# Performance work log

Hardware: AMD Instinct MI355X
Metric: run time of the kernel (lower is better)

## Reference

```python
import jax, jax.numpy as jnp
import numpy as np


def setup_inputs() -> dict:
    key = jax.random.key(0)
    k1, = jax.random.split(key, 1)
    B, H, W, C = 16, 64, 64, 256
    x = jax.random.normal(k1, (B, H, W, C), dtype=jnp.float32)
    gamma = jnp.zeros((1,), dtype=jnp.float32)
    return {"x": x, "gamma": gamma}


def reference(x, gamma):
    B, H, W, C = x.shape
    a = x.reshape(B, H * W, C)                      # [B, HW, C]
    # aTa[b, i, j] = sum_n a[b, n, i] * a[b, n, j]  -> [B, C, C]
    aTa = jnp.einsum('bni,bnj->bij', a, a)
    attn = jax.nn.softmax(aTa, axis=-1)             # softmax over last channel axis
    # aaTa[b, n, j] = sum_i a[b, n, i] * attn[b, i, j]
    aaTa = jnp.einsum('bni,bij->bnj', a, attn)      # [B, HW, C]
    aaTa = aaTa.reshape(B, H, W, C)
    return gamma * aaTa + x
```

## Files before the change

### kernel.cpp

```cpp
#include <hip/hip_runtime.h>
#include <hip/hip_bf16.h>


#define BB 16
#define NN 4096
#define CC 256
#define SPLITK 8
#define KCHUNK (NN / SPLITK)

typedef __attribute__((ext_vector_type(4))) short short4v;
typedef __attribute__((ext_vector_type(8))) short short8v;
typedef __attribute__((ext_vector_type(4))) float floatx4;

__device__ __forceinline__ unsigned short f2bf(float f) {
    unsigned int u = __float_as_uint(f);
    u += 0x7fffu + ((u >> 16) & 1u);
    return (unsigned short)(u >> 16);
}
__device__ __forceinline__ short4v cvt4(floatx4 v) {
    short4v r;
    r[0] = (short)f2bf(v[0]); r[1] = (short)f2bf(v[1]);
    r[2] = (short)f2bf(v[2]); r[3] = (short)f2bf(v[3]);
    return r;
}

__global__ __launch_bounds__(256) void k_transpose(const float* __restrict__ x,
                                                   unsigned short* __restrict__ aT) {
    __shared__ unsigned short tile[64 * 68];
    const int b  = blockIdx.z;
    const int n0 = blockIdx.x * 64;
    const int c0 = blockIdx.y * 64;
    const int t  = threadIdx.x;
    const int q4 = (t & 15) * 4;
    const int tr = t >> 4;

    const float* xb = x + ((size_t)b * NN + n0) * CC + c0;
    for (int r = 0; r < 4; ++r) {
        int row = tr + 16 * r;
        floatx4 v = *(const floatx4*)(xb + (size_t)row * CC + q4);
        *(short4v*)&tile[row * 68 + q4] = cvt4(v);
    }
    __syncthreads();
    unsigned short* aTb = aT + ((size_t)b * CC + c0) * NN + n0;
    for (int r = 0; r < 4; ++r) {
        int c = tr + 16 * r;
        short4v v;
        v[0] = (short)tile[(q4 + 0) * 68 + c];
        v[1] = (short)tile[(q4 + 1) * 68 + c];
        v[2] = (short)tile[(q4 + 2) * 68 + c];
        v[3] = (short)tile[(q4 + 3) * 68 + c];
        *(short4v*)(aTb + (size_t)c * NN + q4) = v;
    }
}

__global__ __launch_bounds__(256) void k_gemm1(const unsigned short* __restrict__ aT,
                                               float* __restrict__ aTa) {
    __shared__ unsigned short Ap[64 * 72];
    __shared__ unsigned short Bp[64 * 72];
    const int b     = blockIdx.z >> 3;
    const int split = blockIdx.z & 7;
    const int i0 = blockIdx.x * 64;
    const int j0 = blockIdx.y * 64;
    const int t  = threadIdx.x;
    const int w  = t >> 6, l = t & 63;
    const int wm = (w >> 1) * 32, wn = (w & 1) * 32;
    const int lk = (l >> 4) * 8;
    const int lm = l & 15;
    const int sc = t >> 4;
    const int sk = (t & 15) * 4;

    const unsigned short* Abase = aT + ((size_t)b * CC + i0) * NN;
    const unsigned short* Bbase = aT + ((size_t)b * CC + j0) * NN;

    floatx4 acc[2][2] = {};
    const int kbeg = split * KCHUNK;
    for (int k0 = kbeg; k0 < kbeg + KCHUNK; k0 += 64) {
        for (int r = 0; r < 4; ++r) {
            int c = sc + 16 * r;
            *(short4v*)&Ap[c * 72 + sk] = *(const short4v*)(Abase + (size_t)c * NN + k0 + sk);
            *(short4v*)&Bp[c * 72 + sk] = *(const short4v*)(Bbase + (size_t)c * NN + k0 + sk);
        }
        __syncthreads();
        for (int ks = 0; ks < 64; ks += 32) {
            short8v af0 = *(const short8v*)&Ap[(wm + 0  + lm) * 72 + ks + lk];
            short8v af1 = *(const short8v*)&Ap[(wm + 16 + lm) * 72 + ks + lk];
            short8v bf0 = *(const short8v*)&Bp[(wn + 0  + lm) * 72 + ks + lk];
            short8v bf1 = *(const short8v*)&Bp[(wn + 16 + lm) * 72 + ks + lk];
            acc[0][0] = __builtin_amdgcn_mfma_f32_16x16x32_bf16(af0, bf0, acc[0][0], 0, 0, 0);
            acc[0][1] = __builtin_amdgcn_mfma_f32_16x16x32_bf16(af0, bf1, acc[0][1], 0, 0, 0);
            acc[1][0] = __builtin_amdgcn_mfma_f32_16x16x32_bf16(af1, bf0, acc[1][0], 0, 0, 0);
            acc[1][1] = __builtin_amdgcn_mfma_f32_16x16x32_bf16(af1, bf1, acc[1][1], 0, 0, 0);
        }
        __syncthreads();
    }
    const int orow = (l >> 4) * 4;
    for (int mt = 0; mt < 2; ++mt)
        for (int nt = 0; nt < 2; ++nt)
            for (int r = 0; r < 4; ++r) {
                int i = i0 + wm + mt * 16 + orow + r;
                int j = j0 + wn + nt * 16 + lm;
                unsafeAtomicAdd(&aTa[((size_t)b * CC + i) * CC + j], acc[mt][nt][r]);
            }
}

__global__ __launch_bounds__(256) void k_softmax(const float* __restrict__ aTa,
                                                 unsigned short* __restrict__ attnT) {
    const int w = threadIdx.x >> 6;
    const int l = threadIdx.x & 63;
    const int row = blockIdx.x * 4 + w;
    const int b = row >> 8;
    const int i = row & 255;
    const float* p = aTa + ((size_t)b * CC + i) * CC;
    float v0 = p[l], v1 = p[l + 64], v2 = p[l + 128], v3 = p[l + 192];
    float m = fmaxf(fmaxf(v0, v1), fmaxf(v2, v3));
    for (int off = 32; off >= 1; off >>= 1) m = fmaxf(m, __shfl_xor(m, off, 64));
    v0 = __expf(v0 - m); v1 = __expf(v1 - m); v2 = __expf(v2 - m); v3 = __expf(v3 - m);
    float s = v0 + v1 + v2 + v3;
    for (int off = 32; off >= 1; off >>= 1) s += __shfl_xor(s, off, 64);
    float rs = 1.0f / s;
    unsigned short* o = attnT + (size_t)b * CC * CC + i;
    o[(size_t)(l +   0) * CC] = f2bf(v0 * rs);
    o[(size_t)(l +  64) * CC] = f2bf(v1 * rs);
    o[(size_t)(l + 128) * CC] = f2bf(v2 * rs);
    o[(size_t)(l + 192) * CC] = f2bf(v3 * rs);
}

__global__ __launch_bounds__(256) void k_gemm2(const float* __restrict__ x,
                                               const unsigned short* __restrict__ attnT,
                                               const float* __restrict__ gamma,
                                               float* __restrict__ out) {
    __shared__ unsigned short At[64 * 72];
    __shared__ unsigned short Bt[64 * 72];
    const int b  = blockIdx.z;
    const int n0 = blockIdx.x * 64;
    const int j0 = blockIdx.y * 64;
    const int t  = threadIdx.x;
    const int w  = t >> 6, l = t & 63;
    const int wm = (w >> 1) * 32, wn = (w & 1) * 32;
    const int lk = (l >> 4) * 8, lm = l & 15;
    const int sc = t >> 4, sk = (t & 15) * 4;

    const float*          Abase = x + ((size_t)b * NN + n0) * CC;
    const unsigned short* Bbase = attnT + ((size_t)b * CC + j0) * CC;

    floatx4 acc[2][2] = {};
    for (int k0 = 0; k0 < CC; k0 += 64) {
        for (int r = 0; r < 4; ++r) {
            int c = sc + 16 * r;
            floatx4 av = *(const floatx4*)(Abase + (size_t)c * CC + k0 + sk);
            *(short4v*)&At[c * 72 + sk] = cvt4(av);
            *(short4v*)&Bt[c * 72 + sk] = *(const short4v*)(Bbase + (size_t)c * CC + k0 + sk);
        }
        __syncthreads();
        for (int ks = 0; ks < 64; ks += 32) {
            short8v af0 = *(const short8v*)&At[(wm + 0  + lm) * 72 + ks + lk];
            short8v af1 = *(const short8v*)&At[(wm + 16 + lm) * 72 + ks + lk];
            short8v bf0 = *(const short8v*)&Bt[(wn + 0  + lm) * 72 + ks + lk];
            short8v bf1 = *(const short8v*)&Bt[(wn + 16 + lm) * 72 + ks + lk];
            acc[0][0] = __builtin_amdgcn_mfma_f32_16x16x32_bf16(af0, bf0, acc[0][0], 0, 0, 0);
            acc[0][1] = __builtin_amdgcn_mfma_f32_16x16x32_bf16(af0, bf1, acc[0][1], 0, 0, 0);
            acc[1][0] = __builtin_amdgcn_mfma_f32_16x16x32_bf16(af1, bf0, acc[1][0], 0, 0, 0);
            acc[1][1] = __builtin_amdgcn_mfma_f32_16x16x32_bf16(af1, bf1, acc[1][1], 0, 0, 0);
        }
        __syncthreads();
    }
    const float g = gamma[0];
    const int orow = (l >> 4) * 4;
    for (int mt = 0; mt < 2; ++mt)
        for (int nt = 0; nt < 2; ++nt)
            for (int r = 0; r < 4; ++r) {
                int nr = n0 + wm + mt * 16 + orow + r;
                int j  = j0 + wn + nt * 16 + lm;
                size_t idx = ((size_t)b * NN + nr) * CC + j;
                out[idx] = g * acc[mt][nt][r] + x[idx];
            }
}

extern "C" void kernel_launch(void* const* d_in, const int* in_sizes, int n_in,
                              void* d_out, int out_size, void* d_ws, size_t ws_size,
                              hipStream_t stream) {
    const float* x     = (const float*)d_in[0];
    const float* gamma = (const float*)d_in[1];
    float* out = (float*)d_out;

    char* ws = (char*)d_ws;
    unsigned short* aT    = (unsigned short*)ws;
    float*          aTa   = (float*)(ws + (size_t)BB * CC * NN * 2);
    unsigned short* attnT = (unsigned short*)(ws + (size_t)BB * CC * NN * 2
                                                 + (size_t)BB * CC * CC * 4);

    hipMemsetAsync(aTa, 0, (size_t)BB * CC * CC * sizeof(float), stream);

    k_transpose<<<dim3(NN / 64, CC / 64, BB), 256, 0, stream>>>(x, aT);
    k_gemm1   <<<dim3(CC / 64, CC / 64, BB * SPLITK), 256, 0, stream>>>(aT, aTa);
    k_softmax <<<dim3(BB * CC / 4),          256, 0, stream>>>(aTa, attnT);
    k_gemm2   <<<dim3(NN / 64, CC / 64, BB), 256, 0, stream>>>(x, attnT, gamma, out);
}
```

Baseline: 187.3 us.

## Widen GEMM tiles to 64x256 and replace split-K atomics with partial buffers

Both GEMMs now compute a 64x256 output tile per block, with each wave owning a 64x64 sub-tile of sixteen accumulators. This cuts redundant reloads of the A operand (x is read once per row block in gemm2) and raises MFMA work per LDS load. Split-K atomics and the memset in gemm1 are replaced by writing per-split partial results to workspace, which softmax then sums. The cost is more LDS per block (about 46KB), more registers, fewer blocks in flight (512 for gemm1, 1024 for gemm2), and eightfold partial-buffer traffic for softmax to read.

```diff
diff --git a/kernel.cpp b/kernel.cpp
--- a/kernel.cpp
+++ b/kernel.cpp
@@ -54,64 +54,80 @@
 }
 
 __global__ __launch_bounds__(256) void k_gemm1(const unsigned short* __restrict__ aT,
-                                               float* __restrict__ aTa) {
+                                               float* __restrict__ part) {
     __shared__ unsigned short Ap[64 * 72];
-    __shared__ unsigned short Bp[64 * 72];
-    const int b     = blockIdx.z >> 3;
-    const int split = blockIdx.z & 7;
-    const int i0 = blockIdx.x * 64;
-    const int j0 = blockIdx.y * 64;
+    __shared__ unsigned short Bp[256 * 72];
+    const int i0    = blockIdx.x * 64;
+    const int b     = blockIdx.y;
+    const int split = blockIdx.z;
     const int t  = threadIdx.x;
     const int w  = t >> 6, l = t & 63;
-    const int wm = (w >> 1) * 32, wn = (w & 1) * 32;
     const int lk = (l >> 4) * 8;
     const int lm = l & 15;
     const int sc = t >> 4;
     const int sk = (t & 15) * 4;
 
     const unsigned short* Abase = aT + ((size_t)b * CC + i0) * NN;
-    const unsigned short* Bbase = aT + ((size_t)b * CC + j0) * NN;
-
-    floatx4 acc[2][2] = {};
+    const unsigned short* Bbase = aT + (size_t)b * CC * NN;
+
+    floatx4 acc[4][4] = {};
     const int kbeg = split * KCHUNK;
     for (int k0 = kbeg; k0 < kbeg + KCHUNK; k0 += 64) {
+        #pragma unroll
         for (int r = 0; r < 4; ++r) {
-            int c = sc + 16 * r;
-            *(short4v*)&Ap[c * 72 + sk] = *(const short4v*)(Abase + (size_t)c * NN + k0 + sk);
-            *(short4v*)&Bp[c * 72 + sk] = *(const short4v*)(Bbase + (size_t)c * NN + k0 + sk);
-        }
-        __syncthreads();
+            int i = sc + 16 * r;
+            *(short4v*)&Ap[i * 72 + sk] = *(const short4v*)(Abase + (size_t)i * NN + k0 + sk);
+        }
+        #pragma unroll
+        for (int r = 0; r < 16; ++r) {
+            int j = sc + 16 * r;
+            *(short4v*)&Bp[j * 72 + sk] = *(const short4v*)(Bbase + (size_t)j * NN + k0 + sk);
+        }
+        __syncthreads();
+        #pragma unroll
         for (int ks = 0; ks < 64; ks += 32) {
-            short8v af0 = *(const short8v*)&Ap[(wm + 0  + lm) * 72 + ks + lk];
-            short8v af1 = *(const short8v*)&Ap[(wm + 16 + lm) * 72 + ks + lk];
-            short8v bf0 = *(const short8v*)&Bp[(wn + 0  + lm) * 72 + ks + lk];
-            short8v bf1 = *(const short8v*)&Bp[(wn + 16 + lm) * 72 + ks + lk];
-            acc[0][0] = __builtin_amdgcn_mfma_f32_16x16x32_bf16(af0, bf0, acc[0][0], 0, 0, 0);
-            acc[0][1] = __builtin_amdgcn_mfma_f32_16x16x32_bf16(af0, bf1, acc[0][1], 0, 0, 0);
-            acc[1][0] = __builtin_amdgcn_mfma_f32_16x16x32_bf16(af1, bf0, acc[1][0], 0, 0, 0);
-            acc[1][1] = __builtin_amdgcn_mfma_f32_16x16x32_bf16(af1, bf1, acc[1][1], 0, 0, 0);
+            short8v af[4], bf[4];
+            #pragma unroll
+            for (int mt = 0; mt < 4; ++mt)
+                af[mt] = *(const short8v*)&Ap[(mt * 16 + lm) * 72 + ks + lk];
+            #pragma unroll
+            for (int nt = 0; nt < 4; ++nt)
+                bf[nt] = *(const short8v*)&Bp[(w * 64 + nt * 16 + lm) * 72 + ks + lk];
+            #pragma unroll
+            for (int mt = 0; mt < 4; ++mt)
+                #pragma unroll
+                for (int nt = 0; nt < 4; ++nt)
+                    acc[mt][nt] = __builtin_amdgcn_mfma_f32_16x16x32_bf16(af[mt], bf[nt], acc[mt][nt], 0, 0, 0);
         }
         __syncthreads();
     }
     const int orow = (l >> 4) * 4;
-    for (int mt = 0; mt < 2; ++mt)
-        for (int nt = 0; nt < 2; ++nt)
+    float* pout = part + ((size_t)(split * BB + b) * CC) * CC;
+    #pragma unroll
+    for (int mt = 0; mt < 4; ++mt)
+        #pragma unroll
+        for (int nt = 0; nt < 4; ++nt)
+            #pragma unroll
             for (int r = 0; r < 4; ++r) {
-                int i = i0 + wm + mt * 16 + orow + r;
-                int j = j0 + wn + nt * 16 + lm;
-                unsafeAtomicAdd(&aTa[((size_t)b * CC + i) * CC + j], acc[mt][nt][r]);
+                int i = i0 + mt * 16 + orow + r;
+                int j = w * 64 + nt * 16 + lm;
+                pout[(size_t)i * CC + j] = acc[mt][nt][r];
             }
 }
 
-__global__ __launch_bounds__(256) void k_softmax(const float* __restrict__ aTa,
+__global__ __launch_bounds__(256) void k_softmax(const float* __restrict__ part,
                                                  unsigned short* __restrict__ attnT) {
     const int w = threadIdx.x >> 6;
     const int l = threadIdx.x & 63;
     const int row = blockIdx.x * 4 + w;
     const int b = row >> 8;
     const int i = row & 255;
-    const float* p = aTa + ((size_t)b * CC + i) * CC;
-    float v0 = p[l], v1 = p[l + 64], v2 = p[l + 128], v3 = p[l + 192];
+    float v0 = 0.f, v1 = 0.f, v2 = 0.f, v3 = 0.f;
+    #pragma unroll
+    for (int s = 0; s < SPLITK; ++s) {
+        const float* p = part + ((size_t)(s * BB + b) * CC + i) * CC;
+        v0 += p[l]; v1 += p[l + 64]; v2 += p[l + 128]; v3 += p[l + 192];
+    }
     float m = fmaxf(fmaxf(v0, v1), fmaxf(v2, v3));
     for (int off = 32; off >= 1; off >>= 1) m = fmaxf(m, __shfl_xor(m, off, 64));
     v0 = __expf(v0 - m); v1 = __expf(v1 - m); v2 = __expf(v2 - m); v3 = __expf(v3 - m);
@@ -130,47 +146,58 @@
                                                const float* __restrict__ gamma,
                                                float* __restrict__ out) {
     __shared__ unsigned short At[64 * 72];
-    __shared__ unsigned short Bt[64 * 72];
-    const int b  = blockIdx.z;
+    __shared__ unsigned short Bt[256 * 72];
     const int n0 = blockIdx.x * 64;
-    const int j0 = blockIdx.y * 64;
+    const int b  = blockIdx.y;
     const int t  = threadIdx.x;
     const int w  = t >> 6, l = t & 63;
-    const int wm = (w >> 1) * 32, wn = (w & 1) * 32;
     const int lk = (l >> 4) * 8, lm = l & 15;
     const int sc = t >> 4, sk = (t & 15) * 4;
 
     const float*          Abase = x + ((size_t)b * NN + n0) * CC;
-    const unsigned short* Bbase = attnT + ((size_t)b * CC + j0) * CC;
-
-    floatx4 acc[2][2] = {};
+    const unsigned short* Bbase = attnT + (size_t)b * CC * CC;
+
+    floatx4 acc[4][4] = {};
     for (int k0 = 0; k0 < CC; k0 += 64) {
+        #pragma unroll
         for (int r = 0; r < 4; ++r) {
-            int c = sc + 16 * r;
-            floatx4 av = *(const floatx4*)(Abase + (size_t)c * CC + k0 + sk);
-            *(short4v*)&At[c * 72 + sk] = cvt4(av);
-            *(short4v*)&Bt[c * 72 + sk] = *(const short4v*)(Bbase + (size_t)c * CC + k0 + sk);
-        }
-        __syncthreads();
+            int n = sc + 16 * r;
+            floatx4 av = *(const floatx4*)(Abase + (size_t)n * CC + k0 + sk);
+            *(short4v*)&At[n * 72 + sk] = cvt4(av);
+        }
+        #pragma unroll
+        for (int r = 0; r < 16; ++r) {
+            int j = sc + 16 * r;
+            *(short4v*)&Bt[j * 72 + sk] = *(const short4v*)(Bbase + (size_t)j * CC + k0 + sk);
+        }
+        __syncthreads();
+        #pragma unroll
         for (int ks = 0; ks < 64; ks += 32) {
-            short8v af0 = *(const short8v*)&At[(wm + 0  + lm) * 72 + ks + lk];
-            short8v af1 = *(const short8v*)&At[(wm + 16 + lm) * 72 + ks + lk];
-            short8v bf0 = *(const short8v*)&Bt[(wn + 0  + lm) * 72 + ks + lk];
-            short8v bf1 = *(const short8v*)&Bt[(wn + 16 + lm) * 72 + ks + lk];
-            acc[0][0] = __builtin_amdgcn_mfma_f32_16x16x32_bf16(af0, bf0, acc[0][0], 0, 0, 0);
-            acc[0][1] = __builtin_amdgcn_mfma_f32_16x16x32_bf16(af0, bf1, acc[0][1], 0, 0, 0);
-            acc[1][0] = __builtin_amdgcn_mfma_f32_16x16x32_bf16(af1, bf0, acc[1][0], 0, 0, 0);
-            acc[1][1] = __builtin_amdgcn_mfma_f32_16x16x32_bf16(af1, bf1, acc[1][1], 0, 0, 0);
+            short8v af[4], bf[4];
+            #pragma unroll
+            for (int mt = 0; mt < 4; ++mt)
+                af[mt] = *(const short8v*)&At[(mt * 16 + lm) * 72 + ks + lk];
+            #pragma unroll
+            for (int nt = 0; nt < 4; ++nt)
+                bf[nt] = *(const short8v*)&Bt[(w * 64 + nt * 16 + lm) * 72 + ks + lk];
+            #pragma unroll
+            for (int mt = 0; mt < 4; ++mt)
+                #pragma unroll
+                for (int nt = 0; nt < 4; ++nt)
+                    acc[mt][nt] = __builtin_amdgcn_mfma_f32_16x16x32_bf16(af[mt], bf[nt], acc[mt][nt], 0, 0, 0);
         }
         __syncthreads();
     }
     const float g = gamma[0];
     const int orow = (l >> 4) * 4;
-    for (int mt = 0; mt < 2; ++mt)
-        for (int nt = 0; nt < 2; ++nt)
+    #pragma unroll
+    for (int mt = 0; mt < 4; ++mt)
+        #pragma unroll
+        for (int nt = 0; nt < 4; ++nt)
+            #pragma unroll
             for (int r = 0; r < 4; ++r) {
-                int nr = n0 + wm + mt * 16 + orow + r;
-                int j  = j0 + wn + nt * 16 + lm;
+                int nr = n0 + mt * 16 + orow + r;
+                int j  = w * 64 + nt * 16 + lm;
                 size_t idx = ((size_t)b * NN + nr) * CC + j;
                 out[idx] = g * acc[mt][nt][r] + x[idx];
             }
@@ -185,14 +212,12 @@
 
     char* ws = (char*)d_ws;
     unsigned short* aT    = (unsigned short*)ws;
-    float*          aTa   = (float*)(ws + (size_t)BB * CC * NN * 2);
+    float*          part  = (float*)(ws + (size_t)BB * CC * NN * 2);
     unsigned short* attnT = (unsigned short*)(ws + (size_t)BB * CC * NN * 2
-                                                 + (size_t)BB * CC * CC * 4);
-
-    hipMemsetAsync(aTa, 0, (size_t)BB * CC * CC * sizeof(float), stream);
+                                                 + (size_t)SPLITK * BB * CC * CC * 4);
 
     k_transpose<<<dim3(NN / 64, CC / 64, BB), 256, 0, stream>>>(x, aT);
-    k_gemm1   <<<dim3(CC / 64, CC / 64, BB * SPLITK), 256, 0, stream>>>(aT, aTa);
-    k_softmax <<<dim3(BB * CC / 4),          256, 0, stream>>>(aTa, attnT);
-    k_gemm2   <<<dim3(NN / 64, CC / 64, BB), 256, 0, stream>>>(x, attnT, gamma, out);
-}
+    k_gemm1   <<<dim3(CC / 64, BB, SPLITK),   256, 0, stream>>>(aT, part);
+    k_softmax <<<dim3(BB * CC / 4),           256, 0, stream>>>(part, attnT);
+    k_gemm2   <<<dim3(NN / 64, BB),           256, 0, stream>>>(x, attnT, gamma, out);
+}
```

New measurement: 180.3 us. 3.8% less time.
